# Optimization experiments

Measured on AMD Instinct MI355X. Metric: run time of the kernel, lower is better.

Reference implementation:

```python
import jax, jax.numpy as jnp
import numpy as np

L, ND, ED, AD = 2, 128, 64, 64
N, E, A, G = 50000, 300000, 600000, 16
EPS = 1e-5


def _graph_norm(h, batch, num_graphs, w, b):
    # PyG LayerNorm(mode='graph'): scalar mean/var over all nodes*features per graph.
    F = h.shape[-1]
    cnt = jax.ops.segment_sum(jnp.ones(h.shape[0], h.dtype), batch, num_segments=num_graphs)
    norm = jnp.maximum(cnt, 1.0) * F  # [G]
    mean = (jax.ops.segment_sum(h, batch, num_segments=num_graphs).sum(-1) / norm)[batch][:, None]
    hc = h - mean
    var = (jax.ops.segment_sum(hc * hc, batch, num_segments=num_graphs).sum(-1) / norm)
    out = hc * jax.lax.rsqrt(var + EPS)[batch][:, None]
    return out * w + b


def setup_inputs() -> dict:
    key = jax.random.key(0)
    ks = jax.random.split(key, 24)

    def lin(k, fi, fo):
        return jax.random.normal(k, (L, fi, fo), jnp.float32) / jnp.sqrt(float(fi))

    inp = {
        "x": jax.random.normal(ks[0], (N, ND), jnp.float32),
        "edge_attr": jax.random.normal(ks[1], (E, ED), jnp.float32),
        "angle_attr": jax.random.normal(ks[2], (A, AD), jnp.float32),
        # node_edge_mlp: [2*ND+ED -> ED], plain linear (plain_last=True)
        "W_ne": lin(ks[3], 2 * ND + ED, ED), "b_ne": jnp.zeros((L, ED), jnp.float32),
        "g_e": jnp.ones((L, ED), jnp.float32), "be_e": jnp.zeros((L, ED), jnp.float32),
        # edge_angle_mlp: [2*ED+AD -> AD]
        "W_ea": lin(ks[4], 2 * ED + AD, AD), "b_ea": jnp.zeros((L, AD), jnp.float32),
        "g_a": jnp.ones((L, AD), jnp.float32), "be_a": jnp.zeros((L, AD), jnp.float32),
        # edge_graph_mp message net: [2*ED+AD -> ED]
        "W_emp": lin(ks[5], 2 * ED + AD, ED), "b_emp": jnp.zeros((L, ED), jnp.float32),
        "g_emp": jnp.ones((L, ED), jnp.float32), "be_emp": jnp.zeros((L, ED), jnp.float32),
        # node_graph_mp message net: [2*ND+ED -> ND]
        "W_nmp": lin(ks[6], 2 * ND + ED, ND), "b_nmp": jnp.zeros((L, ND), jnp.float32),
        "g_nmp": jnp.ones((L, ND), jnp.float32), "be_nmp": jnp.zeros((L, ND), jnp.float32),
        "node_batch": jnp.sort(jax.random.randint(ks[7], (N,), 0, G)),
        "edge_index": jax.random.randint(ks[8], (2, E), 0, N),
        "edge_batch": jnp.sort(jax.random.randint(ks[9], (E,), 0, G)),
        "threebody_index": jax.random.randint(ks[10], (2, A), 0, E),
        "angle_batch": jnp.sort(jax.random.randint(ks[11], (A,), 0, G)),
        "num_graphs": G,
    }
    return inp


def reference(x, edge_attr, angle_attr,
              W_ne, b_ne, g_e, be_e,
              W_ea, b_ea, g_a, be_a,
              W_emp, b_emp, g_emp, be_emp,
              W_nmp, b_nmp, g_nmp, be_nmp,
              node_batch, edge_index, edge_batch,
              threebody_index, angle_batch, num_graphs):
    src_e, dst_e = edge_index[0], edge_index[1]
    src_t, dst_t = threebody_index[0], threebody_index[1]
    n_nodes, n_edges = x.shape[0], edge_attr.shape[0]
    for i in range(W_ne.shape[0]):
        # node-pair -> edge update + residual + graph norm
        ecat = jnp.concatenate([x[src_e], x[dst_e], edge_attr], axis=-1)
        edge_attr = edge_attr + ecat @ W_ne[i] + b_ne[i]
        edge_attr = _graph_norm(edge_attr, edge_batch, num_graphs, g_e[i], be_e[i])
        # edge-pair -> angle update + residual + graph norm
        acat = jnp.concatenate([edge_attr[src_t], edge_attr[dst_t], angle_attr], axis=-1)
        angle_attr = angle_attr + acat @ W_ea[i] + b_ea[i]
        angle_attr = _graph_norm(angle_attr, angle_batch, num_graphs, g_a[i], be_a[i])
        # edge_graph_mp: angle-mediated message passing over edges
        mcat = jnp.concatenate([edge_attr[src_t], edge_attr[dst_t], angle_attr], axis=-1)
        msg = jax.nn.relu(mcat @ W_emp[i] + b_emp[i])
        agg = jax.ops.segment_sum(msg, dst_t, num_segments=n_edges)
        edge_attr = _graph_norm(edge_attr + agg, edge_batch, num_graphs, g_emp[i], be_emp[i])
        # node_graph_mp: edge-mediated message passing over nodes
        ncat = jnp.concatenate([x[src_e], x[dst_e], edge_attr], axis=-1)
        nmsg = jax.nn.relu(ncat @ W_nmp[i] + b_nmp[i])
        nagg = jax.ops.segment_sum(nmsg, dst_e, num_segments=n_nodes)
        x = _graph_norm(x + nagg, node_batch, num_graphs, g_nmp[i], be_nmp[i])
    return x
```

## Files before the change

### kernel.cpp

```cpp
#include <hip/hip_runtime.h>

typedef __attribute__((ext_vector_type(8))) short bf16x8_t;
typedef __attribute__((ext_vector_type(4))) short bf16x4_t;
typedef __attribute__((ext_vector_type(4))) float f32x4_t;

constexpr int NG = 16;
constexpr float EPS = 1e-5f;

__device__ inline unsigned short f2bf(float f) {
  unsigned u = __builtin_bit_cast(unsigned, f);
  u += 0x7FFFu + ((u >> 16) & 1u);
  return (unsigned short)(u >> 16);
}
__device__ inline float bf2f(unsigned short u) {
  unsigned x = ((unsigned)u) << 16;
  return __builtin_bit_cast(float, x);
}

template<bool F32>
__device__ inline void ldrow8(const void* base, size_t off, float v[8]) {
  if constexpr (F32) {
    const float* p = (const float*)base + off;
    float4 f0 = *(const float4*)p, f1 = *(const float4*)(p + 4);
    v[0]=f0.x; v[1]=f0.y; v[2]=f0.z; v[3]=f0.w;
    v[4]=f1.x; v[5]=f1.y; v[6]=f1.z; v[7]=f1.w;
  } else {
    bf16x8_t t = *(const bf16x8_t*)((const unsigned short*)base + off);
#pragma unroll
    for (int k = 0; k < 8; ++k) v[k] = bf2f((unsigned short)t[k]);
  }
}

__global__ __launch_bounds__(256) void k_dense_x(
    const float* __restrict__ x,
    const unsigned short* __restrict__ WtNE,
    const unsigned short* __restrict__ WtNM,
    unsigned short* __restrict__ P, int nN)
{
  int gw = (int)((blockIdx.x * 256u + threadIdx.x) >> 6);
  int ntile = nN >> 4;
  if (gw >= ntile) return;
  int lane = threadIdx.x & 63;
  int colb = lane & 15;
  int ko = (lane >> 4) << 3;
  int rowb = (lane >> 4) << 2;
  int row = (gw << 4) + colb;
  const float* xr = x + (size_t)row * 128;
  f32x4_t a1[4] = {}, a2[4] = {}, a3[8] = {}, a4[8] = {};
#pragma unroll
  for (int c = 0; c < 4; ++c) {
    float4 f0 = *(const float4*)(xr + c * 32 + ko);
    float4 f1 = *(const float4*)(xr + c * 32 + ko + 4);
    float vv[8] = {f0.x,f0.y,f0.z,f0.w,f1.x,f1.y,f1.z,f1.w};
    bf16x8_t a;
#pragma unroll
    for (int k = 0; k < 8; ++k) a[k] = (short)f2bf(vv[k]);
#pragma unroll
    for (int nb = 0; nb < 4; ++nb) {
      bf16x8_t b1 = *(const bf16x8_t*)(WtNE + (size_t)(nb * 16 + colb) * 320 + c * 32 + ko);
      a1[nb] = __builtin_amdgcn_mfma_f32_16x16x32_bf16(a, b1, a1[nb], 0, 0, 0);
      bf16x8_t b2 = *(const bf16x8_t*)(WtNE + (size_t)(nb * 16 + colb) * 320 + (c + 4) * 32 + ko);
      a2[nb] = __builtin_amdgcn_mfma_f32_16x16x32_bf16(a, b2, a2[nb], 0, 0, 0);
    }
#pragma unroll
    for (int nb = 0; nb < 8; ++nb) {
      bf16x8_t b3 = *(const bf16x8_t*)(WtNM + (size_t)(nb * 16 + colb) * 320 + c * 32 + ko);
      a3[nb] = __builtin_amdgcn_mfma_f32_16x16x32_bf16(a, b3, a3[nb], 0, 0, 0);
      bf16x8_t b4 = *(const bf16x8_t*)(WtNM + (size_t)(nb * 16 + colb) * 320 + (c + 4) * 32 + ko);
      a4[nb] = __builtin_amdgcn_mfma_f32_16x16x32_bf16(a, b4, a4[nb], 0, 0, 0);
    }
  }
#pragma unroll
  for (int r = 0; r < 4; ++r) {
    size_t ro = (size_t)((gw << 4) + rowb + r) * 384;
    bf16x4_t t1, t2;
#pragma unroll
    for (int nb = 0; nb < 4; ++nb) { t1[nb] = (short)f2bf(a1[nb][r]); t2[nb] = (short)f2bf(a2[nb][r]); }
    *(bf16x4_t*)(P + ro + colb * 4) = t1;
    *(bf16x4_t*)(P + ro + 64 + colb * 4) = t2;
    bf16x8_t t3, t4;
#pragma unroll
    for (int nb = 0; nb < 8; ++nb) { t3[nb] = (short)f2bf(a3[nb][r]); t4[nb] = (short)f2bf(a4[nb][r]); }
    *(bf16x8_t*)(P + ro + 128 + colb * 8) = t3;
    *(bf16x8_t*)(P + ro + 256 + colb * 8) = t4;
  }
}

__global__ __launch_bounds__(256) void k_prep_e(
    const unsigned short* __restrict__ eA, const int* __restrict__ ebatch,
    const float* __restrict__ afA, const float* __restrict__ afB,
    const unsigned short* __restrict__ WtA,
    const unsigned short* __restrict__ WtP,
    unsigned short* __restrict__ PAE, int nE)
{
  __shared__ float lA[1024], lB[1024];
  for (int i = threadIdx.x; i < 1024; i += 256) { lA[i] = afA[i]; lB[i] = afB[i]; }
  __syncthreads();
  int gw = (int)((blockIdx.x * 256u + threadIdx.x) >> 6);
  int ntile = nE >> 4;
  if (gw >= ntile) return;
  int lane = threadIdx.x & 63;
  int colb = lane & 15;
  int ko = (lane >> 4) << 3;
  int rowb = (lane >> 4) << 2;
  int row = (gw << 4) + colb;
  int ge = ebatch[row];
  f32x4_t pa1[4] = {}, pa2[4] = {}, pe3[4] = {}, pe4[4] = {};
#pragma unroll
  for (int c2 = 0; c2 < 2; ++c2) {
    int fb = c2 * 32 + ko;
    bf16x8_t t = *(const bf16x8_t*)(eA + (size_t)row * 64 + fb);
    bf16x8_t an;
#pragma unroll
    for (int k = 0; k < 8; ++k)
      an[k] = (short)f2bf(bf2f((unsigned short)t[k]) * lA[ge*64 + fb + k] + lB[ge*64 + fb + k]);
#pragma unroll
    for (int nb = 0; nb < 4; ++nb) {
      size_t wb = (size_t)(nb * 16 + colb) * 192;
      bf16x8_t b;
      b = *(const bf16x8_t*)(WtA + wb + c2 * 32 + ko);
      pa1[nb] = __builtin_amdgcn_mfma_f32_16x16x32_bf16(an, b, pa1[nb], 0, 0, 0);
      b = *(const bf16x8_t*)(WtA + wb + 64 + c2 * 32 + ko);
      pa2[nb] = __builtin_amdgcn_mfma_f32_16x16x32_bf16(an, b, pa2[nb], 0, 0, 0);
      b = *(const bf16x8_t*)(WtP + wb + c2 * 32 + ko);
      pe3[nb] = __builtin_amdgcn_mfma_f32_16x16x32_bf16(an, b, pe3[nb], 0, 0, 0);
      b = *(const bf16x8_t*)(WtP + wb + 64 + c2 * 32 + ko);
      pe4[nb] = __builtin_amdgcn_mfma_f32_16x16x32_bf16(an, b, pe4[nb], 0, 0, 0);
    }
  }
#pragma unroll
  for (int r = 0; r < 4; ++r) {
    size_t ro = (size_t)((gw << 4) + rowb + r) * 256;
    bf16x4_t t1, t3, t2, t4;
#pragma unroll
    for (int nb = 0; nb < 4; ++nb) {
      t1[nb] = (short)f2bf(pa1[nb][r]); t3[nb] = (short)f2bf(pe3[nb][r]);
      t2[nb] = (short)f2bf(pa2[nb][r]); t4[nb] = (short)f2bf(pe4[nb][r]);
    }
    *(bf16x4_t*)(PAE + ro + colb * 4) = t1;
    *(bf16x4_t*)(PAE + ro + 64 + colb * 4) = t3;
    *(bf16x4_t*)(PAE + ro + 128 + colb * 4) = t2;
    *(bf16x4_t*)(PAE + ro + 192 + colb * 4) = t4;
  }
}

template<bool EF32>
__global__ __launch_bounds__(256) void k_edge(
    const unsigned short* __restrict__ P, const void* e_in, unsigned short* e_out,
    const int* __restrict__ ei, const int* __restrict__ ebatch,
    const unsigned short* __restrict__ Wt,
    const float* __restrict__ bias,
    const float* __restrict__ afA, const float* __restrict__ afB,
    float* __restrict__ gs1, float* __restrict__ gs2, int nE)
{
  __shared__ float lA[1024], lB[1024];
  __shared__ float ls1[NG], ls2[NG];
  __shared__ __align__(16) unsigned short tl[4][16][72];
  for (int i = threadIdx.x; i < 1024; i += 256) { lA[i] = afA[i]; lB[i] = afB[i]; }
  if (threadIdx.x < NG) { ls1[threadIdx.x] = 0.f; ls2[threadIdx.x] = 0.f; }
  __syncthreads();
  int gw = (int)((blockIdx.x * 256u + threadIdx.x) >> 6);
  int ntile = nE >> 4;
  bool act = gw < ntile;
  int lane = threadIdx.x & 63;
  int wid = threadIdx.x >> 6;
  int colb = lane & 15;
  int ko = (lane >> 4) << 3;
  int rowb = (lane >> 4) << 2;
  float sr[4] = {0.f,0.f,0.f,0.f}, ssr[4] = {0.f,0.f,0.f,0.f};
  if (act) {
    int sI[4], dI[4];
#pragma unroll
    for (int r = 0; r < 4; ++r) {
      int e_r = (gw << 4) + rowb + r;
      sI[r] = ei[e_r]; dI[r] = ei[nE + e_r];
    }
    bf16x4_t g1[4], g2[4];
#pragma unroll
    for (int r = 0; r < 4; ++r) {
      g1[r] = *(const bf16x4_t*)(P + (size_t)sI[r] * 384 + colb * 4);
      g2[r] = *(const bf16x4_t*)(P + (size_t)dI[r] * 384 + 64 + colb * 4);
    }
    int row = (gw << 4) + colb;
    int ge = ebatch[row];
    f32x4_t acc[4] = {};
#pragma unroll
    for (int c2 = 0; c2 < 2; ++c2) {
      int fb = c2 * 32 + ko;
      float vv[8];
      ldrow8<EF32>(e_in, (size_t)row * 64 + fb, vv);
      bf16x8_t a;
#pragma unroll
      for (int k = 0; k < 8; ++k) a[k] = (short)f2bf(vv[k] * lA[ge*64 + fb + k] + lB[ge*64 + fb + k]);
      *(bf16x8_t*)&tl[wid][colb][fb] = a;
#pragma unroll
      for (int nb = 0; nb < 4; ++nb) {
        bf16x8_t b = *(const bf16x8_t*)(Wt + (size_t)(nb * 16 + colb) * 320 + (8 + c2) * 32 + ko);
        acc[nb] = __builtin_amdgcn_mfma_f32_16x16x32_bf16(a, b, acc[nb], 0, 0, 0);
      }
    }
#pragma unroll
    for (int r = 0; r < 4; ++r) {
      int e_ = (gw << 4) + rowb + r;
#pragma unroll
      for (int nb = 0; nb < 4; ++nb) {
        int col = nb * 16 + colb;
        size_t off = (size_t)e_ * 64 + col;
        float nv = bf2f(tl[wid][rowb + r][col]);
        float vv = nv + bias[col]
                 + acc[nb][r] + bf2f((unsigned short)g1[r][nb]) + bf2f((unsigned short)g2[r][nb]);
        e_out[off] = f2bf(vv);
        sr[r] += vv; ssr[r] += vv * vv;
      }
    }
  }
#pragma unroll
  for (int m = 1; m <= 8; m <<= 1)
#pragma unroll
    for (int r = 0; r < 4; ++r) { sr[r] += __shfl_xor(sr[r], m); ssr[r] += __shfl_xor(ssr[r], m); }
  if (act && colb == 0) {
#pragma unroll
    for (int r = 0; r < 4; ++r) {
      int g = ebatch[(gw << 4) + rowb + r];
      atomicAdd(&ls1[g], sr[r]); atomicAdd(&ls2[g], ssr[r]);
    }
  }
  __syncthreads();
  if (threadIdx.x < NG) {
    atomicAdd(&gs1[threadIdx.x], ls1[threadIdx.x]);
    atomicAdd(&gs2[threadIdx.x], ls2[threadIdx.x]);
  }
}

template<bool AF32>
__global__ __launch_bounds__(256) void k_angle(
    const unsigned short* __restrict__ PAE,
    const void* a_in, unsigned short* a_out,
    const int* __restrict__ ti, const int* __restrict__ abatch,
    const unsigned short* __restrict__ Wt,
    const float* __restrict__ bias,
    const float* __restrict__ afAA, const float* __restrict__ afAB,
    float* __restrict__ gs1, float* __restrict__ gs2, int nA)
{
  __shared__ float lAA[1024], lAB[1024];
  __shared__ float ls1[NG], ls2[NG];
  __shared__ __align__(16) unsigned short tl[4][16][72];
  for (int i = threadIdx.x; i < 1024; i += 256) { lAA[i] = afAA[i]; lAB[i] = afAB[i]; }
  if (threadIdx.x < NG) { ls1[threadIdx.x] = 0.f; ls2[threadIdx.x] = 0.f; }
  __syncthreads();
  int gw = (int)((blockIdx.x * 256u + threadIdx.x) >> 6);
  int ntile = nA >> 4;
  bool act = gw < ntile;
  int lane = threadIdx.x & 63;
  int wid = threadIdx.x >> 6;
  int colb = lane & 15;
  int ko = (lane >> 4) << 3;
  int rowb = (lane >> 4) << 2;
  float sr[4] = {0.f,0.f,0.f,0.f}, ssr[4] = {0.f,0.f,0.f,0.f};
  if (act) {
    int sI[4], dI[4];
#pragma unroll
    for (int r = 0; r < 4; ++r) {
      int a_r = (gw << 4) + rowb + r;
      sI[r] = ti[a_r]; dI[r] = ti[nA + a_r];
    }
    bf16x4_t gS[4], gD[4];
#pragma unroll
    for (int r = 0; r < 4; ++r) {
      gS[r] = *(const bf16x4_t*)(PAE + (size_t)sI[r] * 256 + colb * 4);
      gD[r] = *(const bf16x4_t*)(PAE + (size_t)dI[r] * 256 + 128 + colb * 4);
    }
    int row = (gw << 4) + colb;
    int ga = abatch[row];
    f32x4_t acc[4] = {};
#pragma unroll
    for (int c2 = 0; c2 < 2; ++c2) {
      int fb = c2 * 32 + ko;
      float vv[8];
      ldrow8<AF32>(a_in, (size_t)row * 64 + fb, vv);
      bf16x8_t a;
#pragma unroll
      for (int k = 0; k < 8; ++k) a[k] = (short)f2bf(vv[k] * lAA[ga*64 + fb + k] + lAB[ga*64 + fb + k]);
      *(bf16x8_t*)&tl[wid][colb][fb] = a;
#pragma unroll
      for (int nb = 0; nb < 4; ++nb) {
        bf16x8_t b = *(const bf16x8_t*)(Wt + (size_t)(nb * 16 + colb) * 192 + 128 + c2 * 32 + ko);
        acc[nb] = __builtin_amdgcn_mfma_f32_16x16x32_bf16(a, b, acc[nb], 0, 0, 0);
      }
    }
#pragma unroll
    for (int r = 0; r < 4; ++r) {
      int a_ = (gw << 4) + rowb + r;
#pragma unroll
      for (int nb = 0; nb < 4; ++nb) {
        int col = nb * 16 + colb;
        size_t off = (size_t)a_ * 64 + col;
        float nv = bf2f(tl[wid][rowb + r][col]);
        float vv = nv + bias[col] + acc[nb][r]
                 + bf2f((unsigned short)gS[r][nb]) + bf2f((unsigned short)gD[r][nb]);
        a_out[off] = f2bf(vv);
        sr[r] += vv; ssr[r] += vv * vv;
      }
    }
  }
#pragma unroll
  for (int m = 1; m <= 8; m <<= 1)
#pragma unroll
    for (int r = 0; r < 4; ++r) { sr[r] += __shfl_xor(sr[r], m); ssr[r] += __shfl_xor(ssr[r], m); }
  if (act && colb == 0) {
#pragma unroll
    for (int r = 0; r < 4; ++r) {
      int g = abatch[(gw << 4) + rowb + r];
      atomicAdd(&ls1[g], sr[r]); atomicAdd(&ls2[g], ssr[r]);
    }
  }
  __syncthreads();
  if (threadIdx.x < NG) {
    atomicAdd(&gs1[threadIdx.x], ls1[threadIdx.x]);
    atomicAdd(&gs2[threadIdx.x], ls2[threadIdx.x]);
  }
}

__global__ __launch_bounds__(256) void k_fin_emp(
    const unsigned short* __restrict__ PAE,
    const unsigned short* __restrict__ a_, const int* __restrict__ ti,
    const int* __restrict__ abatch, const int* __restrict__ opos,
    const unsigned short* __restrict__ Wt,
    const float* __restrict__ bias,
    const float* __restrict__ afAA, const float* __restrict__ afAB,
    unsigned short* __restrict__ msg, int nA)
{
  __shared__ float lAA[1024], lAB[1024];
  for (int i = threadIdx.x; i < 1024; i += 256) { lAA[i] = afAA[i]; lAB[i] = afAB[i]; }
  __syncthreads();
  int gw = (int)((blockIdx.x * 256u + threadIdx.x) >> 6);
  int ntile = nA >> 4;
  if (gw >= ntile) return;
  int lane = threadIdx.x & 63;
  int colb = lane & 15;
  int ko = (lane >> 4) << 3;
  int rowb = (lane >> 4) << 2;
  int sI[4], dI[4], wr[4];
#pragma unroll
  for (int r = 0; r < 4; ++r) {
    int a_r = (gw << 4) + rowb + r;
    sI[r] = ti[a_r]; dI[r] = ti[nA + a_r]; wr[r] = opos[a_r];
  }
  bf16x4_t g3[4], g4[4];
#pragma unroll
  for (int r = 0; r < 4; ++r) {
    g3[r] = *(const bf16x4_t*)(PAE + (size_t)sI[r] * 256 + 64 + colb * 4);
    g4[r] = *(const bf16x4_t*)(PAE + (size_t)dI[r] * 256 + 192 + colb * 4);
  }
  int row = (gw << 4) + colb;
  int ga = abatch[row];
  f32x4_t acc[4] = {};
#pragma unroll
  for (int c2 = 0; c2 < 2; ++c2) {
    int fb = c2 * 32 + ko;
    bf16x8_t t = *(const bf16x8_t*)(a_ + (size_t)row * 64 + fb);
    bf16x8_t a;
#pragma unroll
    for (int k = 0; k < 8; ++k)
      a[k] = (short)f2bf(bf2f((unsigned short)t[k]) * lAA[ga*64 + fb + k] + lAB[ga*64 + fb + k]);
#pragma unroll
    for (int nb = 0; nb < 4; ++nb) {
      bf16x8_t b = *(const bf16x8_t*)(Wt + (size_t)(nb * 16 + colb) * 192 + 128 + c2 * 32 + ko);
      acc[nb] = __builtin_amdgcn_mfma_f32_16x16x32_bf16(a, b, acc[nb], 0, 0, 0);
    }
  }
#pragma unroll
  for (int r = 0; r < 4; ++r) {
#pragma unroll
    for (int nb = 0; nb < 4; ++nb) {
      int col = nb * 16 + colb;
      float v = fmaxf(acc[nb][r] + bf2f((unsigned short)g3[r][nb]) + bf2f((unsigned short)g4[r][nb])
                      + bias[col], 0.f);
      msg[(size_t)wr[r] * 64 + col] = f2bf(v);
    }
  }
}

__global__ __launch_bounds__(256) void k_fin_nmp(
    const unsigned short* __restrict__ P,
    const unsigned short* __restrict__ e, const int* __restrict__ ei,
    const int* __restrict__ ebatch, const int* __restrict__ opos,
    const unsigned short* __restrict__ Wt,
    const float* __restrict__ bias,
    const float* __restrict__ afEA, const float* __restrict__ afEB,
    unsigned short* __restrict__ msg, int nE)
{
  __shared__ float lEA[1024], lEB[1024];
  for (int i = threadIdx.x; i < 1024; i += 256) { lEA[i] = afEA[i]; lEB[i] = afEB[i]; }
  __syncthreads();
  int gw = (int)((blockIdx.x * 256u + threadIdx.x) >> 6);
  int ntile = nE >> 4;
  if (gw >= ntile) return;
  int lane = threadIdx.x & 63;
  int colb = lane & 15;
  int ko = (lane >> 4) << 3;
  int rowb = (lane >> 4) << 2;
  int sI[4], dI[4], wr[4];
#pragma unroll
  for (int r = 0; r < 4; ++r) {
    int e_r = (gw << 4) + rowb + r;
    sI[r] = ei[e_r]; dI[r] = ei[nE + e_r]; wr[r] = opos[e_r];
  }
  bf16x8_t g3[4], g4[4];
#pragma unroll
  for (int r = 0; r < 4; ++r) {
    g3[r] = *(const bf16x8_t*)(P + (size_t)sI[r] * 384 + 128 + colb * 8);
    g4[r] = *(const bf16x8_t*)(P + (size_t)dI[r] * 384 + 256 + colb * 8);
  }
  int row = (gw << 4) + colb;
  int ge = ebatch[row];
  f32x4_t acc[8] = {};
#pragma unroll
  for (int c2 = 0; c2 < 2; ++c2) {
    int fb = c2 * 32 + ko;
    bf16x8_t t = *(const bf16x8_t*)(e + (size_t)row * 64 + fb);
    bf16x8_t a;
#pragma unroll
    for (int k = 0; k < 8; ++k)
      a[k] = (short)f2bf(bf2f((unsigned short)t[k]) * lEA[ge*64 + fb + k] + lEB[ge*64 + fb + k]);
#pragma unroll
    for (int nb = 0; nb < 8; ++nb) {
      bf16x8_t b = *(const bf16x8_t*)(Wt + (size_t)(nb * 16 + colb) * 320 + (8 + c2) * 32 + ko);
      acc[nb] = __builtin_amdgcn_mfma_f32_16x16x32_bf16(a, b, acc[nb], 0, 0, 0);
    }
  }
#pragma unroll
  for (int r = 0; r < 4; ++r) {
#pragma unroll
    for (int nb = 0; nb < 8; ++nb) {
      int col = nb * 16 + colb;
      float v = fmaxf(acc[nb][r] + bf2f((unsigned short)g3[r][nb]) + bf2f((unsigned short)g4[r][nb])
                      + bias[col], 0.f);
      msg[(size_t)wr[r] * 128 + col] = f2bf(v);
    }
  }
}

__global__ __launch_bounds__(256) void k_red_e(
    const unsigned short* __restrict__ msg, const unsigned short* e_in, unsigned short* e_out,
    const int* __restrict__ ptr, const int* __restrict__ ebatch,
    const float* __restrict__ afA, const float* __restrict__ afB,
    float* __restrict__ gs1, float* __restrict__ gs2, int nE)
{
  __shared__ float lA[1024], lB[1024], ls1[NG], ls2[NG];
  for (int i = threadIdx.x; i < 1024; i += 256) { lA[i] = afA[i]; lB[i] = afB[i]; }
  if (threadIdx.x < NG) { ls1[threadIdx.x] = 0.f; ls2[threadIdx.x] = 0.f; }
  __syncthreads();
  int lane = threadIdx.x & 63;
  int wv = (int)((blockIdx.x * 256u + threadIdx.x) >> 6);
  int nw = (int)((gridDim.x * 256u) >> 6);
  for (int eidx = wv; eidx < nE; eidx += nw) {
    int p0 = ptr[eidx], p1 = ptr[eidx + 1];
    float sum = 0.f;
    for (int j = p0; j < p1; ++j)
      sum += bf2f(msg[(size_t)j * 64 + lane]);
    int g = ebatch[eidx];
    size_t off = (size_t)eidx * 64 + lane;
    float v = bf2f(e_in[off]) * lA[g*64 + lane] + lB[g*64 + lane] + sum;
    e_out[off] = f2bf(v);
    float s = v, ss = v * v;
#pragma unroll
    for (int m = 1; m < 64; m <<= 1) { s += __shfl_xor(s, m); ss += __shfl_xor(ss, m); }
    if (lane == 0) { atomicAdd(&ls1[g], s); atomicAdd(&ls2[g], ss); }
  }
  __syncthreads();
  if (threadIdx.x < NG) {
    atomicAdd(&gs1[threadIdx.x], ls1[threadIdx.x]);
    atomicAdd(&gs2[threadIdx.x], ls2[threadIdx.x]);
  }
}

__global__ __launch_bounds__(256) void k_red_n(
    const unsigned short* __restrict__ msg, const float* x_in, float* out,
    const int* __restrict__ ptr, const int* __restrict__ nbatch,
    float* __restrict__ gs1, float* __restrict__ gs2, int nN)
{
  __shared__ float ls1[NG], ls2[NG];
  if (threadIdx.x < NG) { ls1[threadIdx.x] = 0.f; ls2[threadIdx.x] = 0.f; }
  __syncthreads();
  int lane = threadIdx.x & 63;
  int wv = (int)((blockIdx.x * 256u + threadIdx.x) >> 6);
  int nw = (int)((gridDim.x * 256u) >> 6);
  for (int n = wv; n < nN; n += nw) {
    int p0 = ptr[n], p1 = ptr[n + 1];
    float s0 = 0.f, s1v = 0.f;
    for (int j = p0; j < p1; ++j) {
      unsigned u = *(const unsigned*)(msg + (size_t)j * 128 + lane * 2);
      s0 += bf2f((unsigned short)(u & 0xffffu));
      s1v += bf2f((unsigned short)(u >> 16));
    }
    size_t off = (size_t)n * 128 + lane * 2;
    float h0 = x_in[off] + s0, h1 = x_in[off + 1] + s1v;
    out[off] = h0; out[off + 1] = h1;
    float s = h0 + h1, ss = h0 * h0 + h1 * h1;
#pragma unroll
    for (int m = 1; m < 64; m <<= 1) { s += __shfl_xor(s, m); ss += __shfl_xor(ss, m); }
    if (lane == 0) { int g = nbatch[n]; atomicAdd(&ls1[g], s); atomicAdd(&ls2[g], ss); }
  }
  __syncthreads();
  if (threadIdx.x < NG) {
    atomicAdd(&gs1[threadIdx.x], ls1[threadIdx.x]);
    atomicAdd(&gs2[threadIdx.x], ls2[threadIdx.x]);
  }
}

__global__ __launch_bounds__(256) void k_mkaff(
    const float* __restrict__ s1, const float* __restrict__ s2,
    const float* __restrict__ cnt, int F,
    const float* __restrict__ w, const float* __restrict__ b,
    float* __restrict__ A, float* __restrict__ B)
{
  int idx = blockIdx.x * 256 + threadIdx.x;
  if (idx >= NG * F) return;
  int g = idx / F, f = idx - g * F;
  float norm = fmaxf(cnt[g], 1.f) * (float)F;
  float m = s1[g] / norm;
  float var = s2[g] / norm - m * m;
  float inv = rsqrtf(var + EPS);
  float a = inv * w[f];
  A[idx] = a;
  B[idx] = b[f] - m * a;
}

__global__ __launch_bounds__(256) void k_idaff(float* __restrict__ A, float* __restrict__ B, int n)
{
  int idx = blockIdx.x * 256 + threadIdx.x;
  if (idx < n) { A[idx] = 1.f; B[idx] = 0.f; }
}

__global__ __launch_bounds__(256) void k_apply(
    float* h, const int* __restrict__ batch,
    const float* __restrict__ A, const float* __restrict__ B, int nN)
{
  int total = nN * 16;
  int stride = gridDim.x * 256;
  for (int idx = blockIdx.x * 256 + threadIdx.x; idx < total; idx += stride) {
    int row = idx >> 4, q = (idx & 15) * 8;
    int g = batch[row];
    float* hp = h + (size_t)row * 128 + q;
    float4 f0 = *(const float4*)hp;
    float4 f1 = *(const float4*)(hp + 4);
    float vv[8] = {f0.x,f0.y,f0.z,f0.w,f1.x,f1.y,f1.z,f1.w};
#pragma unroll
    for (int k = 0; k < 8; ++k) vv[k] = vv[k] * A[(g << 7) + q + k] + B[(g << 7) + q + k];
    float4 g0 = {vv[0],vv[1],vv[2],vv[3]}, g1 = {vv[4],vv[5],vv[6],vv[7]};
    *(float4*)hp = g0;
    *(float4*)(hp + 4) = g1;
  }
}

__global__ __launch_bounds__(256) void k_count(
    const int* __restrict__ batch, int n, float* __restrict__ cnt)
{
  __shared__ float lc[NG];
  if (threadIdx.x < NG) lc[threadIdx.x] = 0.f;
  __syncthreads();
  for (int i = blockIdx.x * 256 + threadIdx.x; i < n; i += gridDim.x * 256)
    atomicAdd(&lc[batch[i]], 1.f);
  __syncthreads();
  if (threadIdx.x < NG) atomicAdd(&cnt[threadIdx.x], lc[threadIdx.x]);
}

__global__ __launch_bounds__(256) void k_hist(
    const int* __restrict__ dst, int n, int* __restrict__ cnt)
{
  for (int i = blockIdx.x * 256 + threadIdx.x; i < n; i += gridDim.x * 256)
    atomicAdd(&cnt[dst[i]], 1);
}

__global__ __launch_bounds__(256) void k_scan1(
    const int* __restrict__ in, int* __restrict__ out, int* __restrict__ bsum, int n)
{
  __shared__ int wtot[4];
  int tid = threadIdx.x, lane = tid & 63, wid = tid >> 6;
  int base = blockIdx.x * 1024 + tid * 4;
  int v[4];
#pragma unroll
  for (int k = 0; k < 4; ++k) v[k] = (base + k < n) ? in[base + k] : 0;
  int tsum = v[0] + v[1] + v[2] + v[3];
  int incl = tsum;
#pragma unroll
  for (int off = 1; off < 64; off <<= 1) {
    int up = __shfl_up(incl, off);
    if (lane >= off) incl += up;
  }
  if (lane == 63) wtot[wid] = incl;
  __syncthreads();
  if (tid == 0) {
    int r = 0;
#pragma unroll
    for (int w2 = 0; w2 < 4; ++w2) { int t = wtot[w2]; wtot[w2] = r; r += t; }
    bsum[blockIdx.x] = r;
  }
  __syncthreads();
  int excl = wtot[wid] + incl - tsum;
#pragma unroll
  for (int k = 0; k < 4; ++k) {
    if (base + k < n) out[base + k] = excl;
    excl += v[k];
  }
}

__global__ __launch_bounds__(256) void k_scan2(int* __restrict__ bsum, int nb, int* __restrict__ total_out)
{
  __shared__ int wtot[4];
  int tid = threadIdx.x, lane = tid & 63, wid = tid >> 6;
  int base = tid * 4;
  int v[4];
#pragma unroll
  for (int k = 0; k < 4; ++k) v[k] = (base + k < nb) ? bsum[base + k] : 0;
  int tsum = v[0] + v[1] + v[2] + v[3];
  int incl = tsum;
#pragma unroll
  for (int off = 1; off < 64; off <<= 1) {
    int up = __shfl_up(incl, off);
    if (lane >= off) incl += up;
  }
  if (lane == 63) wtot[wid] = incl;
  __syncthreads();
  if (tid == 0) {
    int r = 0;
#pragma unroll
    for (int w2 = 0; w2 < 4; ++w2) { int t = wtot[w2]; wtot[w2] = r; r += t; }
    *total_out = r;
  }
  __syncthreads();
  int excl = wtot[wid] + incl - tsum;
#pragma unroll
  for (int k = 0; k < 4; ++k) {
    if (base + k < nb) bsum[base + k] = excl;
    excl += v[k];
  }
}

__global__ __launch_bounds__(256) void k_scan3(
    int* __restrict__ ptr, int* __restrict__ cur, const int* __restrict__ bsum, int n)
{
  for (int i = blockIdx.x * 256 + threadIdx.x; i < n; i += gridDim.x * 256) {
    int v = ptr[i] + bsum[i >> 10];
    ptr[i] = v; cur[i] = v;
  }
}

__global__ __launch_bounds__(256) void k_scatter(
    const int* __restrict__ dst, int* __restrict__ cur, int* __restrict__ perm, int n)
{
  for (int i = blockIdx.x * 256 + threadIdx.x; i < n; i += gridDim.x * 256) {
    int d = dst[i];
    int p = atomicAdd(&cur[d], 1);
    perm[p] = i;
  }
}

__global__ __launch_bounds__(256) void k_invperm(
    const int* __restrict__ perm, int* __restrict__ opos, int n)
{
  for (int j = blockIdx.x * 256 + threadIdx.x; j < n; j += gridDim.x * 256)
    opos[perm[j]] = j;
}

__global__ __launch_bounds__(256) void k_wt(
    const float* __restrict__ W, unsigned short* __restrict__ Wt, int K, int NO)
{
  int idx = blockIdx.x * 256 + threadIdx.x;
  if (idx >= K * NO) return;
  int k = idx / NO, j = idx - k * NO;
  Wt[(size_t)j * K + k] = f2bf(W[idx]);
}

extern "C" void kernel_launch(void* const* d_in, const int* in_sizes, int n_in,
                              void* d_out, int out_size, void* d_ws, size_t ws_size,
                              hipStream_t stream)
{
  const float* x0    = (const float*)d_in[0];
  const float* e0    = (const float*)d_in[1];
  const float* a0    = (const float*)d_in[2];
  const float* W_ne  = (const float*)d_in[3];
  const float* b_ne  = (const float*)d_in[4];
  const float* g_e   = (const float*)d_in[5];
  const float* be_e  = (const float*)d_in[6];
  const float* W_ea  = (const float*)d_in[7];
  const float* b_ea  = (const float*)d_in[8];
  const float* g_a   = (const float*)d_in[9];
  const float* be_a  = (const float*)d_in[10];
  const float* W_emp = (const float*)d_in[11];
  const float* b_emp = (const float*)d_in[12];
  const float* g_emp = (const float*)d_in[13];
  const float* be_emp= (const float*)d_in[14];
  const float* W_nmp = (const float*)d_in[15];
  const float* b_nmp = (const float*)d_in[16];
  const float* g_nmp = (const float*)d_in[17];
  const float* be_nmp= (const float*)d_in[18];
  const int* node_batch  = (const int*)d_in[19];
  const int* edge_index  = (const int*)d_in[20];
  const int* edge_batch  = (const int*)d_in[21];
  const int* tb_index    = (const int*)d_in[22];
  const int* angle_batch = (const int*)d_in[23];

  const int N = in_sizes[0] / 128;
  const int E = in_sizes[1] / 64;
  const int A = in_sizes[2] / 64;

  char* wsp = (char*)d_ws;
  auto alloc = [&](size_t bytes) { char* p = wsp; wsp += (bytes + 255) & ~(size_t)255; return p; };
  unsigned short* eAB  = (unsigned short*)alloc((size_t)E * 64 * 2);
  unsigned short* aAB  = (unsigned short*)alloc((size_t)A * 64 * 2);
  unsigned short* msg  = (unsigned short*)alloc((size_t)A * 64 * 2);
  unsigned short* P    = (unsigned short*)alloc((size_t)N * 384 * 2);
  unsigned short* PAE  = (unsigned short*)alloc((size_t)E * 256 * 2);
  int* ptr_n  = (int*)alloc((size_t)(N + 1) * 4);
  int* cur_n  = (int*)alloc((size_t)N * 4);
  int* perm_n = (int*)alloc((size_t)E * 4);
  int* ptr_e  = (int*)alloc((size_t)(E + 1) * 4);
  int* cur_e  = (int*)alloc((size_t)E * 4);
  int* perm_e = (int*)alloc((size_t)A * 4);
  int* opos_n = (int*)alloc((size_t)E * 4);
  int* opos_e = (int*)alloc((size_t)A * 4);
  int* bsum   = (int*)alloc(4096 * 4);
  float* stats = (float*)alloc(5 * NG * 4);
  float* s1    = stats;
  float* s2    = stats + NG;
  float* cnt_n = stats + 2 * NG;
  float* cnt_e = stats + 3 * NG;
  float* cnt_a = stats + 4 * NG;
  float* afE_idA = (float*)alloc(1024 * 4); float* afE_idB = (float*)alloc(1024 * 4);
  float* afA_idA = (float*)alloc(1024 * 4); float* afA_idB = (float*)alloc(1024 * 4);
  float* afE1A   = (float*)alloc(1024 * 4); float* afE1B   = (float*)alloc(1024 * 4);
  float* afE2A   = (float*)alloc(1024 * 4); float* afE2B   = (float*)alloc(1024 * 4);
  float* afA1A   = (float*)alloc(1024 * 4); float* afA1B   = (float*)alloc(1024 * 4);
  float* afXA    = (float*)alloc(2048 * 4); float* afXB    = (float*)alloc(2048 * 4);
  unsigned short* wt_ne  = (unsigned short*)alloc((size_t)2 * 320 * 64 * 2);
  unsigned short* wt_ea  = (unsigned short*)alloc((size_t)2 * 192 * 64 * 2);
  unsigned short* wt_emp = (unsigned short*)alloc((size_t)2 * 192 * 64 * 2);
  unsigned short* wt_nmp = (unsigned short*)alloc((size_t)2 * 320 * 128 * 2);

  float* x_out = (float*)d_out;

  for (int i = 0; i < 2; ++i) {
    k_wt<<<(320*64 + 255)/256, 256, 0, stream>>>(W_ne  + (size_t)i*320*64,  wt_ne  + (size_t)i*320*64,  320, 64);
    k_wt<<<(192*64 + 255)/256, 256, 0, stream>>>(W_ea  + (size_t)i*192*64,  wt_ea  + (size_t)i*192*64,  192, 64);
    k_wt<<<(192*64 + 255)/256, 256, 0, stream>>>(W_emp + (size_t)i*192*64,  wt_emp + (size_t)i*192*64,  192, 64);
    k_wt<<<(320*128 + 255)/256, 256, 0, stream>>>(W_nmp + (size_t)i*320*128, wt_nmp + (size_t)i*320*128, 320, 128);
  }
  hipMemsetAsync(stats, 0, 5 * NG * 4, stream);
  k_count<<<512, 256, 0, stream>>>(node_batch, N, cnt_n);
  k_count<<<512, 256, 0, stream>>>(edge_batch, E, cnt_e);
  k_count<<<512, 256, 0, stream>>>(angle_batch, A, cnt_a);
  k_idaff<<<4, 256, 0, stream>>>(afE_idA, afE_idB, 1024);
  k_idaff<<<4, 256, 0, stream>>>(afA_idA, afA_idB, 1024);

  hipMemsetAsync(cur_n, 0, (size_t)N * 4, stream);
  hipMemsetAsync(cur_e, 0, (size_t)E * 4, stream);
  k_hist<<<1024, 256, 0, stream>>>(edge_index + E, E, cur_n);
  k_hist<<<1024, 256, 0, stream>>>(tb_index + A, A, cur_e);
  int nbN = (N + 1023) / 1024, nbE = (E + 1023) / 1024;
  k_scan1<<<nbN, 256, 0, stream>>>(cur_n, ptr_n, bsum, N);
  k_scan2<<<1, 256, 0, stream>>>(bsum, nbN, ptr_n + N);
  k_scan3<<<1024, 256, 0, stream>>>(ptr_n, cur_n, bsum, N);
  k_scatter<<<1024, 256, 0, stream>>>(edge_index + E, cur_n, perm_n, E);
  k_invperm<<<1024, 256, 0, stream>>>(perm_n, opos_n, E);
  k_scan1<<<nbE, 256, 0, stream>>>(cur_e, ptr_e, bsum, E);
  k_scan2<<<1, 256, 0, stream>>>(bsum, nbE, ptr_e + E);
  k_scan3<<<1024, 256, 0, stream>>>(ptr_e, cur_e, bsum, E);
  k_scatter<<<1024, 256, 0, stream>>>(tb_index + A, cur_e, perm_e, A);
  k_invperm<<<1024, 256, 0, stream>>>(perm_e, opos_e, A);

  const float* x_cur = x0;
  int blkE = (E / 16 + 3) / 4;
  int blkA = (A / 16 + 3) / 4;
  int blkN = (N / 16 + 3) / 4;

  for (int i = 0; i < 2; ++i) {
    const float* fEinA = (i == 0) ? afE_idA : afE2A;
    const float* fEinB = (i == 0) ? afE_idB : afE2B;
    const float* fAinA = (i == 0) ? afA_idA : afA1A;
    const float* fAinB = (i == 0) ? afA_idB : afA1B;

    k_dense_x<<<blkN, 256, 0, stream>>>(x_cur, wt_ne + (size_t)i*320*64,
                                        wt_nmp + (size_t)i*320*128, P, N);

    hipMemsetAsync(s1, 0, 2 * NG * 4, stream);
    if (i == 0)
      k_edge<true><<<blkE, 256, 0, stream>>>(P, (const void*)e0, eAB, edge_index, edge_batch,
                                             wt_ne + (size_t)i*320*64, b_ne + i*64,
                                             fEinA, fEinB, s1, s2, E);
    else
      k_edge<false><<<blkE, 256, 0, stream>>>(P, (const void*)eAB, eAB, edge_index, edge_batch,
                                              wt_ne + (size_t)i*320*64, b_ne + i*64,
                                              fEinA, fEinB, s1, s2, E);
    k_mkaff<<<4, 256, 0, stream>>>(s1, s2, cnt_e, 64, g_e + i*64, be_e + i*64, afE1A, afE1B);

    k_prep_e<<<blkE, 256, 0, stream>>>(eAB, edge_batch, afE1A, afE1B,
                                       wt_ea + (size_t)i*192*64, wt_emp + (size_t)i*192*64,
                                       PAE, E);

    hipMemsetAsync(s1, 0, 2 * NG * 4, stream);
    if (i == 0)
      k_angle<true><<<blkA, 256, 0, stream>>>(PAE, (const void*)a0, aAB, tb_index, angle_batch,
                                              wt_ea + (size_t)i*192*64, b_ea + i*64,
                                              fAinA, fAinB, s1, s2, A);
    else
      k_angle<false><<<blkA, 256, 0, stream>>>(PAE, (const void*)aAB, aAB, tb_index, angle_batch,
                                               wt_ea + (size_t)i*192*64, b_ea + i*64,
                                               fAinA, fAinB, s1, s2, A);
    k_mkaff<<<4, 256, 0, stream>>>(s1, s2, cnt_a, 64, g_a + i*64, be_a + i*64, afA1A, afA1B);

    k_fin_emp<<<blkA, 256, 0, stream>>>(PAE, aAB, tb_index, angle_batch, opos_e,
                                        wt_emp + (size_t)i*192*64, b_emp + i*64,
                                        afA1A, afA1B, msg, A);
    hipMemsetAsync(s1, 0, 2 * NG * 4, stream);
    k_red_e<<<2048, 256, 0, stream>>>(msg, eAB, eAB, ptr_e, edge_batch,
                                      afE1A, afE1B, s1, s2, E);
    k_mkaff<<<4, 256, 0, stream>>>(s1, s2, cnt_e, 64, g_emp + i*64, be_emp + i*64, afE2A, afE2B);

    k_fin_nmp<<<blkE, 256, 0, stream>>>(P, eAB, edge_index, edge_batch, opos_n,
                                        wt_nmp + (size_t)i*320*128, b_nmp + i*128,
                                        afE2A, afE2B, msg, E);
    hipMemsetAsync(s1, 0, 2 * NG * 4, stream);
    k_red_n<<<2048, 256, 0, stream>>>(msg, x_cur, x_out, ptr_n, node_batch,
                                      s1, s2, N);
    k_mkaff<<<8, 256, 0, stream>>>(s1, s2, cnt_n, 128, g_nmp + i*128, be_nmp + i*128, afXA, afXB);
    k_apply<<<2048, 256, 0, stream>>>(x_out, node_batch, afXA, afXB, N);

    x_cur = x_out;
  }
}
```

Measured before the change: 1.585 ms.

## Fold graph-norm affine computation into consumer kernels and drop intermediate launches

Removes the separate k_mkaff and k_idaff launches and the per-stage stat memsets. Each consumer kernel now computes the per-graph scale and shift into LDS directly from the raw sums, counts and gamma/beta. Each stage gets its own preallocated stats slot, zeroed once up front. The layer-0 node norm is applied inside layer-1's dense and reduce kernels, so only the final k_apply remains. This cuts launch count and small serialized kernels, at the cost of redundant per-block affine setup work, including 2048-entry tables for the node path.

```diff
diff --git a/kernel.cpp b/kernel.cpp
--- a/kernel.cpp
+++ b/kernel.cpp
@@ -15,6 +15,25 @@
 __device__ inline float bf2f(unsigned short u) {
   unsigned x = ((unsigned)u) << 16;
   return __builtin_bit_cast(float, x);
+}
+
+__device__ inline void mkaff_lds(float* lA, float* lB,
+    const float* s1, const float* s2, const float* cnt,
+    const float* gamma, const float* beta, int F, int tid) {
+  int total = NG * F;
+  for (int i = tid; i < total; i += 256) {
+    float a = 1.f, b = 0.f;
+    if (gamma != nullptr) {
+      int g = i / F, f = i - g * F;
+      float norm = fmaxf(cnt[g], 1.f) * (float)F;
+      float m = s1[g] / norm;
+      float var = s2[g] / norm - m * m;
+      float inv = rsqrtf(var + EPS);
+      a = inv * gamma[f];
+      b = beta[f] - m * a;
+    }
+    lA[i] = a; lB[i] = b;
+  }
 }
 
 template<bool F32>
@@ -31,12 +50,21 @@
   }
 }
 
+template<bool APX>
 __global__ __launch_bounds__(256) void k_dense_x(
-    const float* __restrict__ x,
+    const float* __restrict__ x, const int* __restrict__ nbatch,
+    const float* __restrict__ s1, const float* __restrict__ s2,
+    const float* __restrict__ cnt,
+    const float* __restrict__ gm, const float* __restrict__ bt,
     const unsigned short* __restrict__ WtNE,
     const unsigned short* __restrict__ WtNM,
     unsigned short* __restrict__ P, int nN)
 {
+  __shared__ float lA[APX ? 2048 : 1], lB[APX ? 2048 : 1];
+  if (APX) {
+    mkaff_lds(lA, lB, s1, s2, cnt, gm, bt, 128, threadIdx.x);
+    __syncthreads();
+  }
   int gw = (int)((blockIdx.x * 256u + threadIdx.x) >> 6);
   int ntile = nN >> 4;
   if (gw >= ntile) return;
@@ -45,6 +73,7 @@
   int ko = (lane >> 4) << 3;
   int rowb = (lane >> 4) << 2;
   int row = (gw << 4) + colb;
+  int gx = APX ? nbatch[row] : 0;
   const float* xr = x + (size_t)row * 128;
   f32x4_t a1[4] = {}, a2[4] = {}, a3[8] = {}, a4[8] = {};
 #pragma unroll
@@ -54,7 +83,11 @@
     float vv[8] = {f0.x,f0.y,f0.z,f0.w,f1.x,f1.y,f1.z,f1.w};
     bf16x8_t a;
 #pragma unroll
-    for (int k = 0; k < 8; ++k) a[k] = (short)f2bf(vv[k]);
+    for (int k = 0; k < 8; ++k) {
+      float v = vv[k];
+      if (APX) v = v * lA[(gx << 7) + c * 32 + ko + k] + lB[(gx << 7) + c * 32 + ko + k];
+      a[k] = (short)f2bf(v);
+    }
 #pragma unroll
     for (int nb = 0; nb < 4; ++nb) {
       bf16x8_t b1 = *(const bf16x8_t*)(WtNE + (size_t)(nb * 16 + colb) * 320 + c * 32 + ko);
@@ -88,13 +121,15 @@
 
 __global__ __launch_bounds__(256) void k_prep_e(
     const unsigned short* __restrict__ eA, const int* __restrict__ ebatch,
-    const float* __restrict__ afA, const float* __restrict__ afB,
+    const float* __restrict__ s1, const float* __restrict__ s2,
+    const float* __restrict__ cnt,
+    const float* __restrict__ gm, const float* __restrict__ bt,
     const unsigned short* __restrict__ WtA,
     const unsigned short* __restrict__ WtP,
     unsigned short* __restrict__ PAE, int nE)
 {
   __shared__ float lA[1024], lB[1024];
-  for (int i = threadIdx.x; i < 1024; i += 256) { lA[i] = afA[i]; lB[i] = afB[i]; }
+  mkaff_lds(lA, lB, s1, s2, cnt, gm, bt, 64, threadIdx.x);
   __syncthreads();
   int gw = (int)((blockIdx.x * 256u + threadIdx.x) >> 6);
   int ntile = nE >> 4;
@@ -148,15 +183,17 @@
 __global__ __launch_bounds__(256) void k_edge(
     const unsigned short* __restrict__ P, const void* e_in, unsigned short* e_out,
     const int* __restrict__ ei, const int* __restrict__ ebatch,
+    const float* __restrict__ is1, const float* __restrict__ is2,
+    const float* __restrict__ icnt,
+    const float* __restrict__ igm, const float* __restrict__ ibt,
     const unsigned short* __restrict__ Wt,
     const float* __restrict__ bias,
-    const float* __restrict__ afA, const float* __restrict__ afB,
     float* __restrict__ gs1, float* __restrict__ gs2, int nE)
 {
   __shared__ float lA[1024], lB[1024];
   __shared__ float ls1[NG], ls2[NG];
   __shared__ __align__(16) unsigned short tl[4][16][72];
-  for (int i = threadIdx.x; i < 1024; i += 256) { lA[i] = afA[i]; lB[i] = afB[i]; }
+  mkaff_lds(lA, lB, is1, is2, icnt, igm, ibt, 64, threadIdx.x);
   if (threadIdx.x < NG) { ls1[threadIdx.x] = 0.f; ls2[threadIdx.x] = 0.f; }
   __syncthreads();
   int gw = (int)((blockIdx.x * 256u + threadIdx.x) >> 6);
@@ -237,15 +274,17 @@
     const unsigned short* __restrict__ PAE,
     const void* a_in, unsigned short* a_out,
     const int* __restrict__ ti, const int* __restrict__ abatch,
+    const float* __restrict__ is1, const float* __restrict__ is2,
+    const float* __restrict__ icnt,
+    const float* __restrict__ igm, const float* __restrict__ ibt,
     const unsigned short* __restrict__ Wt,
     const float* __restrict__ bias,
-    const float* __restrict__ afAA, const float* __restrict__ afAB,
     float* __restrict__ gs1, float* __restrict__ gs2, int nA)
 {
   __shared__ float lAA[1024], lAB[1024];
   __shared__ float ls1[NG], ls2[NG];
   __shared__ __align__(16) unsigned short tl[4][16][72];
-  for (int i = threadIdx.x; i < 1024; i += 256) { lAA[i] = afAA[i]; lAB[i] = afAB[i]; }
+  mkaff_lds(lAA, lAB, is1, is2, icnt, igm, ibt, 64, threadIdx.x);
   if (threadIdx.x < NG) { ls1[threadIdx.x] = 0.f; ls2[threadIdx.x] = 0.f; }
   __syncthreads();
   int gw = (int)((blockIdx.x * 256u + threadIdx.x) >> 6);
@@ -325,13 +364,15 @@
     const unsigned short* __restrict__ PAE,
     const unsigned short* __restrict__ a_, const int* __restrict__ ti,
     const int* __restrict__ abatch, const int* __restrict__ opos,
+    const float* __restrict__ is1, const float* __restrict__ is2,
+    const float* __restrict__ icnt,
+    const float* __restrict__ igm, const float* __restrict__ ibt,
     const unsigned short* __restrict__ Wt,
     const float* __restrict__ bias,
-    const float* __restrict__ afAA, const float* __restrict__ afAB,
     unsigned short* __restrict__ msg, int nA)
 {
   __shared__ float lAA[1024], lAB[1024];
-  for (int i = threadIdx.x; i < 1024; i += 256) { lAA[i] = afAA[i]; lAB[i] = afAB[i]; }
+  mkaff_lds(lAA, lAB, is1, is2, icnt, igm, ibt, 64, threadIdx.x);
   __syncthreads();
   int gw = (int)((blockIdx.x * 256u + threadIdx.x) >> 6);
   int ntile = nA >> 4;
@@ -385,13 +426,15 @@
     const unsigned short* __restrict__ P,
     const unsigned short* __restrict__ e, const int* __restrict__ ei,
     const int* __restrict__ ebatch, const int* __restrict__ opos,
+    const float* __restrict__ is1, const float* __restrict__ is2,
+    const float* __restrict__ icnt,
+    const float* __restrict__ igm, const float* __restrict__ ibt,
     const unsigned short* __restrict__ Wt,
     const float* __restrict__ bias,
-    const float* __restrict__ afEA, const float* __restrict__ afEB,
     unsigned short* __restrict__ msg, int nE)
 {
   __shared__ float lEA[1024], lEB[1024];
-  for (int i = threadIdx.x; i < 1024; i += 256) { lEA[i] = afEA[i]; lEB[i] = afEB[i]; }
+  mkaff_lds(lEA, lEB, is1, is2, icnt, igm, ibt, 64, threadIdx.x);
   __syncthreads();
   int gw = (int)((blockIdx.x * 256u + threadIdx.x) >> 6);
   int ntile = nE >> 4;
@@ -444,11 +487,13 @@
 __global__ __launch_bounds__(256) void k_red_e(
     const unsigned short* __restrict__ msg, const unsigned short* e_in, unsigned short* e_out,
     const int* __restrict__ ptr, const int* __restrict__ ebatch,
-    const float* __restrict__ afA, const float* __restrict__ afB,
+    const float* __restrict__ is1, const float* __restrict__ is2,
+    const float* __restrict__ icnt,
+    const float* __restrict__ igm, const float* __restrict__ ibt,
     float* __restrict__ gs1, float* __restrict__ gs2, int nE)
 {
   __shared__ float lA[1024], lB[1024], ls1[NG], ls2[NG];
-  for (int i = threadIdx.x; i < 1024; i += 256) { lA[i] = afA[i]; lB[i] = afB[i]; }
+  mkaff_lds(lA, lB, is1, is2, icnt, igm, ibt, 64, threadIdx.x);
   if (threadIdx.x < NG) { ls1[threadIdx.x] = 0.f; ls2[threadIdx.x] = 0.f; }
   __syncthreads();
   int lane = threadIdx.x & 63;
@@ -475,12 +520,18 @@
   }
 }
 
+template<bool APX>
 __global__ __launch_bounds__(256) void k_red_n(
     const unsigned short* __restrict__ msg, const float* x_in, float* out,
     const int* __restrict__ ptr, const int* __restrict__ nbatch,
+    const float* __restrict__ is1, const float* __restrict__ is2,
+    const float* __restrict__ icnt,
+    const float* __restrict__ igm, const float* __restrict__ ibt,
     float* __restrict__ gs1, float* __restrict__ gs2, int nN)
 {
+  __shared__ float lA[APX ? 2048 : 1], lB[APX ? 2048 : 1];
   __shared__ float ls1[NG], ls2[NG];
+  if (APX) mkaff_lds(lA, lB, is1, is2, icnt, igm, ibt, 128, threadIdx.x);
   if (threadIdx.x < NG) { ls1[threadIdx.x] = 0.f; ls2[threadIdx.x] = 0.f; }
   __syncthreads();
   int lane = threadIdx.x & 63;
@@ -494,13 +545,19 @@
       s0 += bf2f((unsigned short)(u & 0xffffu));
       s1v += bf2f((unsigned short)(u >> 16));
     }
+    int g = nbatch[n];
     size_t off = (size_t)n * 128 + lane * 2;
-    float h0 = x_in[off] + s0, h1 = x_in[off + 1] + s1v;
+    float x0v = x_in[off], x1v = x_in[off + 1];
+    if (APX) {
+      x0v = x0v * lA[(g << 7) + lane * 2] + lB[(g << 7) + lane * 2];
+      x1v = x1v * lA[(g << 7) + lane * 2 + 1] + lB[(g << 7) + lane * 2 + 1];
+    }
+    float h0 = x0v + s0, h1 = x1v + s1v;
     out[off] = h0; out[off + 1] = h1;
     float s = h0 + h1, ss = h0 * h0 + h1 * h1;
 #pragma unroll
     for (int m = 1; m < 64; m <<= 1) { s += __shfl_xor(s, m); ss += __shfl_xor(ss, m); }
-    if (lane == 0) { int g = nbatch[n]; atomicAdd(&ls1[g], s); atomicAdd(&ls2[g], ss); }
+    if (lane == 0) { atomicAdd(&ls1[g], s); atomicAdd(&ls2[g], ss); }
   }
   __syncthreads();
   if (threadIdx.x < NG) {
@@ -509,34 +566,15 @@
   }
 }
 
-__global__ __launch_bounds__(256) void k_mkaff(
-    const float* __restrict__ s1, const float* __restrict__ s2,
-    const float* __restrict__ cnt, int F,
-    const float* __restrict__ w, const float* __restrict__ b,
-    float* __restrict__ A, float* __restrict__ B)
-{
-  int idx = blockIdx.x * 256 + threadIdx.x;
-  if (idx >= NG * F) return;
-  int g = idx / F, f = idx - g * F;
-  float norm = fmaxf(cnt[g], 1.f) * (float)F;
-  float m = s1[g] / norm;
-  float var = s2[g] / norm - m * m;
-  float inv = rsqrtf(var + EPS);
-  float a = inv * w[f];
-  A[idx] = a;
-  B[idx] = b[f] - m * a;
-}
-
-__global__ __launch_bounds__(256) void k_idaff(float* __restrict__ A, float* __restrict__ B, int n)
-{
-  int idx = blockIdx.x * 256 + threadIdx.x;
-  if (idx < n) { A[idx] = 1.f; B[idx] = 0.f; }
-}
-
 __global__ __launch_bounds__(256) void k_apply(
     float* h, const int* __restrict__ batch,
-    const float* __restrict__ A, const float* __restrict__ B, int nN)
-{
+    const float* __restrict__ is1, const float* __restrict__ is2,
+    const float* __restrict__ icnt,
+    const float* __restrict__ igm, const float* __restrict__ ibt, int nN)
+{
+  __shared__ float lA[2048], lB[2048];
+  mkaff_lds(lA, lB, is1, is2, icnt, igm, ibt, 128, threadIdx.x);
+  __syncthreads();
   int total = nN * 16;
   int stride = gridDim.x * 256;
   for (int idx = blockIdx.x * 256 + threadIdx.x; idx < total; idx += stride) {
@@ -547,7 +585,7 @@
     float4 f1 = *(const float4*)(hp + 4);
     float vv[8] = {f0.x,f0.y,f0.z,f0.w,f1.x,f1.y,f1.z,f1.w};
 #pragma unroll
-    for (int k = 0; k < 8; ++k) vv[k] = vv[k] * A[(g << 7) + q + k] + B[(g << 7) + q + k];
+    for (int k = 0; k < 8; ++k) vv[k] = vv[k] * lA[(g << 7) + q + k] + lB[(g << 7) + q + k];
     float4 g0 = {vv[0],vv[1],vv[2],vv[3]}, g1 = {vv[4],vv[5],vv[6],vv[7]};
     *(float4*)hp = g0;
     *(float4*)(hp + 4) = g1;
@@ -722,18 +760,11 @@
   int* opos_n = (int*)alloc((size_t)E * 4);
   int* opos_e = (int*)alloc((size_t)A * 4);
   int* bsum   = (int*)alloc(4096 * 4);
-  float* stats = (float*)alloc(5 * NG * 4);
-  float* s1    = stats;
-  float* s2    = stats + NG;
-  float* cnt_n = stats + 2 * NG;
-  float* cnt_e = stats + 3 * NG;
-  float* cnt_a = stats + 4 * NG;
-  float* afE_idA = (float*)alloc(1024 * 4); float* afE_idB = (float*)alloc(1024 * 4);
-  float* afA_idA = (float*)alloc(1024 * 4); float* afA_idB = (float*)alloc(1024 * 4);
-  float* afE1A   = (float*)alloc(1024 * 4); float* afE1B   = (float*)alloc(1024 * 4);
-  float* afE2A   = (float*)alloc(1024 * 4); float* afE2B   = (float*)alloc(1024 * 4);
-  float* afA1A   = (float*)alloc(1024 * 4); float* afA1B   = (float*)alloc(1024 * 4);
-  float* afXA    = (float*)alloc(2048 * 4); float* afXB    = (float*)alloc(2048 * 4);
+  float* stats = (float*)alloc((8 * 2 + 3) * NG * 4);
+  auto stp = [&](int l, int k) { return stats + (size_t)((l * 4 + k) * 2) * NG; };
+  float* cnt_n = stats + 16 * NG;
+  float* cnt_e = stats + 17 * NG;
+  float* cnt_a = stats + 18 * NG;
   unsigned short* wt_ne  = (unsigned short*)alloc((size_t)2 * 320 * 64 * 2);
   unsigned short* wt_ea  = (unsigned short*)alloc((size_t)2 * 192 * 64 * 2);
   unsigned short* wt_emp = (unsigned short*)alloc((size_t)2 * 192 * 64 * 2);
@@ -747,12 +778,10 @@
     k_wt<<<(192*64 + 255)/256, 256, 0, stream>>>(W_emp + (size_t)i*192*64,  wt_emp + (size_t)i*192*64,  192, 64);
     k_wt<<<(320*128 + 255)/256, 256, 0, stream>>>(W_nmp + (size_t)i*320*128, wt_nmp + (size_t)i*320*128, 320, 128);
   }
-  hipMemsetAsync(stats, 0, 5 * NG * 4, stream);
+  hipMemsetAsync(stats, 0, (8 * 2 + 3) * NG * 4, stream);
   k_count<<<512, 256, 0, stream>>>(node_batch, N, cnt_n);
   k_count<<<512, 256, 0, stream>>>(edge_batch, E, cnt_e);
   k_count<<<512, 256, 0, stream>>>(angle_batch, A, cnt_a);
-  k_idaff<<<4, 256, 0, stream>>>(afE_idA, afE_idB, 1024);
-  k_idaff<<<4, 256, 0, stream>>>(afA_idA, afA_idB, 1024);
 
   hipMemsetAsync(cur_n, 0, (size_t)N * 4, stream);
   hipMemsetAsync(cur_e, 0, (size_t)E * 4, stream);
@@ -770,63 +799,75 @@
   k_scatter<<<1024, 256, 0, stream>>>(tb_index + A, cur_e, perm_e, A);
   k_invperm<<<1024, 256, 0, stream>>>(perm_e, opos_e, A);
 
-  const float* x_cur = x0;
   int blkE = (E / 16 + 3) / 4;
   int blkA = (A / 16 + 3) / 4;
   int blkN = (N / 16 + 3) / 4;
 
   for (int i = 0; i < 2; ++i) {
-    const float* fEinA = (i == 0) ? afE_idA : afE2A;
-    const float* fEinB = (i == 0) ? afE_idB : afE2B;
-    const float* fAinA = (i == 0) ? afA_idA : afA1A;
-    const float* fAinB = (i == 0) ? afA_idB : afA1B;
-
-    k_dense_x<<<blkN, 256, 0, stream>>>(x_cur, wt_ne + (size_t)i*320*64,
-                                        wt_nmp + (size_t)i*320*128, P, N);
-
-    hipMemsetAsync(s1, 0, 2 * NG * 4, stream);
+    const float* egm = (i == 0) ? nullptr : g_emp;
+    const float* ebt = (i == 0) ? nullptr : be_emp;
+    const float* es1 = (i == 0) ? nullptr : stp(0, 2);
+    const float* es2 = (i == 0) ? nullptr : stp(0, 2) + NG;
+    const float* agm = (i == 0) ? nullptr : g_a;
+    const float* abt = (i == 0) ? nullptr : be_a;
+    const float* as1 = (i == 0) ? nullptr : stp(0, 1);
+    const float* as2 = (i == 0) ? nullptr : stp(0, 1) + NG;
+
+    if (i == 0)
+      k_dense_x<false><<<blkN, 256, 0, stream>>>(x0, node_batch,
+          nullptr, nullptr, nullptr, nullptr, nullptr,
+          wt_ne, wt_nmp, P, N);
+    else
+      k_dense_x<true><<<blkN, 256, 0, stream>>>(x_out, node_batch,
+          stp(0, 3), stp(0, 3) + NG, cnt_n, g_nmp, be_nmp,
+          wt_ne + (size_t)320*64, wt_nmp + (size_t)320*128, P, N);
+
     if (i == 0)
       k_edge<true><<<blkE, 256, 0, stream>>>(P, (const void*)e0, eAB, edge_index, edge_batch,
-                                             wt_ne + (size_t)i*320*64, b_ne + i*64,
-                                             fEinA, fEinB, s1, s2, E);
+          es1, es2, cnt_e, egm, ebt,
+          wt_ne + (size_t)i*320*64, b_ne + i*64,
+          stp(i, 0), stp(i, 0) + NG, E);
     else
       k_edge<false><<<blkE, 256, 0, stream>>>(P, (const void*)eAB, eAB, edge_index, edge_batch,
-                                              wt_ne + (size_t)i*320*64, b_ne + i*64,
-                                              fEinA, fEinB, s1, s2, E);
-    k_mkaff<<<4, 256, 0, stream>>>(s1, s2, cnt_e, 64, g_e + i*64, be_e + i*64, afE1A, afE1B);
-
-    k_prep_e<<<blkE, 256, 0, stream>>>(eAB, edge_batch, afE1A, afE1B,
-                                       wt_ea + (size_t)i*192*64, wt_emp + (size_t)i*192*64,
-                                       PAE, E);
-
-    hipMemsetAsync(s1, 0, 2 * NG * 4, stream);
+          es1, es2, cnt_e, egm, ebt,
+          wt_ne + (size_t)i*320*64, b_ne + i*64,
+          stp(i, 0), stp(i, 0) + NG, E);
+
+    k_prep_e<<<blkE, 256, 0, stream>>>(eAB, edge_batch,
+        stp(i, 0), stp(i, 0) + NG, cnt_e, g_e + i*64, be_e + i*64,
+        wt_ea + (size_t)i*192*64, wt_emp + (size_t)i*192*64, PAE, E);
+
     if (i == 0)
       k_angle<true><<<blkA, 256, 0, stream>>>(PAE, (const void*)a0, aAB, tb_index, angle_batch,
-                                              wt_ea + (size_t)i*192*64, b_ea + i*64,
-                                              fAinA, fAinB, s1, s2, A);
+          as1, as2, cnt_a, agm, abt,
+          wt_ea + (size_t)i*192*64, b_ea + i*64,
+          stp(i, 1), stp(i, 1) + NG, A);
     else
       k_angle<false><<<blkA, 256, 0, stream>>>(PAE, (const void*)aAB, aAB, tb_index, angle_batch,
-                                               wt_ea + (size_t)i*192*64, b_ea + i*64,
-                                               fAinA, fAinB, s1, s2, A);
-    k_mkaff<<<4, 256, 0, stream>>>(s1, s2, cnt_a, 64, g_a + i*64, be_a + i*64, afA1A, afA1B);
+          as1, as2, cnt_a, agm, abt,
+          wt_ea + (size_t)i*192*64, b_ea + i*64,
+          stp(i, 1), stp(i, 1) + NG, A);
 
     k_fin_emp<<<blkA, 256, 0, stream>>>(PAE, aAB, tb_index, angle_batch, opos_e,
-                                        wt_emp + (size_t)i*192*64, b_emp + i*64,
-                                        afA1A, afA1B, msg, A);
-    hipMemsetAsync(s1, 0, 2 * NG * 4, stream);
+        stp(i, 1), stp(i, 1) + NG, cnt_a, g_a + i*64, be_a + i*64,
+        wt_emp + (size_t)i*192*64, b_emp + i*64, msg, A);
     k_red_e<<<2048, 256, 0, stream>>>(msg, eAB, eAB, ptr_e, edge_batch,
-                                      afE1A, afE1B, s1, s2, E);
-    k_mkaff<<<4, 256, 0, stream>>>(s1, s2, cnt_e, 64, g_emp + i*64, be_emp + i*64, afE2A, afE2B);
+        stp(i, 0), stp(i, 0) + NG, cnt_e, g_e + i*64, be_e + i*64,
+        stp(i, 2), stp(i, 2) + NG, E);
 
     k_fin_nmp<<<blkE, 256, 0, stream>>>(P, eAB, edge_index, edge_batch, opos_n,
-                                        wt_nmp + (size_t)i*320*128, b_nmp + i*128,
-                                        afE2A, afE2B, msg, E);
-    hipMemsetAsync(s1, 0, 2 * NG * 4, stream);
-    k_red_n<<<2048, 256, 0, stream>>>(msg, x_cur, x_out, ptr_n, node_batch,
-                                      s1, s2, N);
-    k_mkaff<<<8, 256, 0, stream>>>(s1, s2, cnt_n, 128, g_nmp + i*128, be_nmp + i*128, afXA, afXB);
-    k_apply<<<2048, 256, 0, stream>>>(x_out, node_batch, afXA, afXB, N);
-
-    x_cur = x_out;
-  }
-}
+        stp(i, 2), stp(i, 2) + NG, cnt_e, g_emp + i*64, be_emp + i*64,
+        wt_nmp + (size_t)i*320*128, b_nmp + i*128, msg, E);
+    if (i == 0)
+      k_red_n<false><<<2048, 256, 0, stream>>>(msg, x0, x_out, ptr_n, node_batch,
+          nullptr, nullptr, nullptr, nullptr, nullptr,
+          stp(i, 3), stp(i, 3) + NG, N);
+    else
+      k_red_n<true><<<2048, 256, 0, stream>>>(msg, x_out, x_out, ptr_n, node_batch,
+          stp(0, 3), stp(0, 3) + NG, cnt_n, g_nmp, be_nmp,
+          stp(i, 3), stp(i, 3) + NG, N);
+  }
+
+  k_apply<<<2048, 256, 0, stream>>>(x_out, node_batch,
+      stp(1, 3), stp(1, 3) + NG, cnt_n, g_nmp + 128, be_nmp + 128, N);
+}
```

Result: faster. 1.551 ms (-2.1%).
